# Performance work log

Hardware: AMD Instinct MI355X
Metric: run time of the kernel (lower is better)

## Reference

```python
import jax, jax.numpy as jnp
import numpy as np
from functools import lru_cache
from jax.scipy.linalg import expm

N_QUBITS = 6
DIM = 2 ** N_QUBITS          # 64
N_PAULI = 4 ** N_QUBITS      # 4096


@lru_cache(maxsize=None)
def _pauli_tensor_np(n_qubits):
    # All n-qubit Pauli strings as dense matrices, ordered base-4
    # (digit 0..3 -> I, X, Y, Z; most-significant digit = first qubit).
    I = np.eye(2, dtype=np.complex64)
    X = np.array([[0, 1], [1, 0]], dtype=np.complex64)
    Y = np.array([[0, -1j], [1j, 0]], dtype=np.complex64)
    Z = np.array([[1, 0], [0, -1]], dtype=np.complex64)
    base = np.stack([I, X, Y, Z])  # [4,2,2]
    T = base
    for _ in range(n_qubits - 1):
        k, d = T.shape[0], T.shape[1]
        T = np.einsum('iab,jcd->ijacbd', T, base).reshape(k * 4, d * 2, d * 2)
    return np.ascontiguousarray(T.astype(np.complex64))  # [4^n, 2^n, 2^n]


def setup_inputs() -> dict:
    key = jax.random.key(0)
    kx, kw, kb = jax.random.split(key, 3)
    x = jax.random.normal(kx, (512, 4000), dtype=jnp.float32)
    weight = jax.random.normal(kw, (4, N_PAULI - 1), dtype=jnp.float32)
    bias = jax.random.normal(kb, (DIM,), dtype=jnp.float32)
    return {"x": x, "weight": weight, "bias": bias}


def reference(x, weight, bias):
    # x: [B, in_dim] float32; weight: [n_reps, 4^n - 1]; bias: [out_dim]
    B, in_dim = x.shape
    n_reps = weight.shape[0]
    out_dim = bias.shape[0]
    P = jnp.asarray(_pauli_tensor_np(N_QUBITS))  # [4096, 64, 64] complex64

    # Pad data coefficients up to the full Pauli basis (identity included).
    xp = jnp.pad(x, ((0, 0), (0, N_PAULI - in_dim))).astype(jnp.complex64)

    # Data-encoding Hamiltonian per sample: H_d[b] = sum_p x[b,p] * P[p]
    Hd = jnp.einsum('bp,pij->bij', xp, P)                       # [B,64,64]
    Ud = jax.vmap(expm)(-1j * Hd)                               # [B,64,64]

    # Trainable Hamiltonians per rep (identity Pauli excluded -> global phase).
    Hp = jnp.einsum('rp,pij->rij', weight.astype(jnp.complex64), P[1:])
    Up = jax.vmap(expm)(-1j * Hp)                               # [R,64,64]

    # Data re-uploading circuit on |0...0>: repeat (U_param @ U_data).
    psi = jnp.zeros((B, DIM), dtype=jnp.complex64).at[:, 0].set(1.0)
    for r in range(n_reps):
        psi = jnp.einsum('bij,bj->bi', Ud, psi)
        psi = jnp.einsum('ij,bj->bi', Up[r], psi)

    # Observables are computational-basis projectors |k><k|, k < out_dim:
    # <psi|O_k|psi> = |psi_k|^2
    probs = (psi[:, :out_dim].real ** 2 + psi[:, :out_dim].imag ** 2)
    return probs.astype(jnp.float32) + bias
```

## Files before the change

### kernel.cpp

```cpp
#include <hip/hip_runtime.h>
#include <math.h>

typedef float2 cplx;
typedef __attribute__((ext_vector_type(8))) short short8v;
typedef __attribute__((ext_vector_type(4))) short short4v;
typedef __attribute__((ext_vector_type(4))) float float4v;

#define TPB 256
#define IN_DIM 4000
#define NREPS 4

#define C3f  0.16666667f
#define C4f  0.041666668f
#define C5f  8.3333333e-3f
#define C6f  1.3888889e-3f
#define C7f  1.9841270e-4f
#define C8f  2.4801587e-5f
#define C9f  2.7557319e-6f
#define C10f 2.7557319e-7f
#define C11f 2.5052108e-8f
#define C12f 2.0876757e-9f
#define C13f 1.6059044e-10f

#define MFMA(A,B,C) __builtin_amdgcn_mfma_f32_16x16x32_bf16((A),(B),(C),0,0,0)


__device__ __forceinline__ int idxSw(int a, int b) {
    return (a << 6) + ((((b >> 3) + a) & 7) << 3) + (b & 7);
}
__device__ __forceinline__ short f2bf(float f) {
    unsigned u = __float_as_uint(f);
    return (short)((u + 0x7FFF + ((u >> 16) & 1)) >> 16);
}
__device__ __forceinline__ float bf2f(short s) {
    return __uint_as_float(((unsigned)(unsigned short)s) << 16);
}

__device__ __forceinline__ void mm_mfma(const short* __restrict__ sh, int li, int q,
                                        int mh, int nh,
                                        float4v* __restrict__ accRR, float4v* __restrict__ accII,
                                        float4v* __restrict__ accRI, float4v* __restrict__ accIR)
{
    #pragma unroll
    for (int ks = 0; ks < 2; ks++) {
        const int ch = ks * 4 + q;
        short8v A[2][4];
        #pragma unroll
        for (int dm = 0; dm < 2; dm++) {
            int r = ((mh * 2 + dm) << 4) + li;
            int off = (r << 6) + (((ch + r) & 7) << 3);
            #pragma unroll
            for (int p = 0; p < 4; p++)
                A[dm][p] = *(const short8v*)(sh + p * 4096 + off);
        }
        #pragma unroll
        for (int dn = 0; dn < 2; dn++) {
            int n = ((nh * 2 + dn) << 4) + li;
            int off = (n << 6) + (((ch + n) & 7) << 3);
            short8v Brh = *(const short8v*)(sh + 16384 + off);
            short8v Brl = *(const short8v*)(sh + 16384 + 4096 + off);
            short8v Bih = *(const short8v*)(sh + 16384 + 8192 + off);
            short8v Bil = *(const short8v*)(sh + 16384 + 12288 + off);
            #pragma unroll
            for (int dm = 0; dm < 2; dm++) {
                int ti = dm * 2 + dn;
                short8v arh = A[dm][0], arl = A[dm][1];
                short8v aih = A[dm][2], ail = A[dm][3];
                accRR[ti] = MFMA(arh, Brh, accRR[ti]);
                accRR[ti] = MFMA(arh, Brl, accRR[ti]);
                accRR[ti] = MFMA(arl, Brh, accRR[ti]);
                accII[ti] = MFMA(aih, Bih, accII[ti]);
                accII[ti] = MFMA(aih, Bil, accII[ti]);
                accII[ti] = MFMA(ail, Bih, accII[ti]);
                accRI[ti] = MFMA(arh, Bih, accRI[ti]);
                accRI[ti] = MFMA(arh, Bil, accRI[ti]);
                accRI[ti] = MFMA(arl, Bih, accRI[ti]);
                accIR[ti] = MFMA(aih, Brh, accIR[ti]);
                accIR[ti] = MFMA(aih, Brl, accIR[ti]);
                accIR[ti] = MFMA(ail, Brh, accIR[ti]);
            }
        }
    }
}

__device__ __forceinline__ void write_row(short* __restrict__ sh, int li, int q,
                                          int mh, int nh,
                                          const float4v* cre, const float4v* cim)
{
    #pragma unroll
    for (int dm = 0; dm < 2; dm++)
    #pragma unroll
    for (int dn = 0; dn < 2; dn++) {
        int ti = dm * 2 + dn;
        int c = ((nh * 2 + dn) << 4) + li;
        #pragma unroll
        for (int reg = 0; reg < 4; reg++) {
            int r = ((mh * 2 + dm) << 4) + q * 4 + reg;
            int off = idxSw(r, c);
            float vr = cre[ti][reg], vi = cim[ti][reg];
            short rh = f2bf(vr); short rl = f2bf(vr - bf2f(rh));
            short ih = f2bf(vi); short il = f2bf(vi - bf2f(ih));
            sh[off] = rh; sh[4096 + off] = rl;
            sh[8192 + off] = ih; sh[12288 + off] = il;
        }
    }
}

__device__ __forceinline__ void write_col(short* __restrict__ sh, int li, int q,
                                          int mh, int nh,
                                          const float4v* cre, const float4v* cim)
{
    #pragma unroll
    for (int dm = 0; dm < 2; dm++)
    #pragma unroll
    for (int dn = 0; dn < 2; dn++) {
        int ti = dm * 2 + dn;
        int c = ((nh * 2 + dn) << 4) + li;
        int k0 = ((mh * 2 + dm) << 4) + q * 4;
        int off = idxSw(c, k0);
        short4v rh, rl, ih, il;
        #pragma unroll
        for (int reg = 0; reg < 4; reg++) {
            float vr = cre[ti][reg], vi = cim[ti][reg];
            short h1 = f2bf(vr); rh[reg] = h1; rl[reg] = f2bf(vr - bf2f(h1));
            short h2 = f2bf(vi); ih[reg] = h2; il[reg] = f2bf(vi - bf2f(h2));
        }
        *(short4v*)(sh + 16384 + off) = rh;
        *(short4v*)(sh + 16384 + 4096 + off) = rl;
        *(short4v*)(sh + 16384 + 8192 + off) = ih;
        *(short4v*)(sh + 16384 + 12288 + off) = il;
    }
}

__device__ __forceinline__ void gather_tile(const short* __restrict__ sh, int li, int q,
                                            int mh, int nh, float4v* bre, float4v* bim)
{
    #pragma unroll
    for (int dm = 0; dm < 2; dm++)
    #pragma unroll
    for (int dn = 0; dn < 2; dn++) {
        int ti = dm * 2 + dn;
        int c = ((nh * 2 + dn) << 4) + li;
        #pragma unroll
        for (int reg = 0; reg < 4; reg++) {
            int r = ((mh * 2 + dm) << 4) + q * 4 + reg;
            int off = idxSw(r, c);
            bre[ti][reg] = bf2f(sh[off]) + bf2f(sh[4096 + off]);
            bim[ti][reg] = bf2f(sh[8192 + off]) + bf2f(sh[12288 + off]);
        }
    }
}

__device__ __forceinline__ void adddiag(float4v* ure, float cI, int li, int q, int mh, int nh)
{
    #pragma unroll
    for (int dm = 0; dm < 2; dm++)
    #pragma unroll
    for (int dn = 0; dn < 2; dn++) {
        if (2 * mh + dm == 2 * nh + dn) {
            #pragma unroll
            for (int e = 0; e < 4; e++)
                if (li == q * 4 + e) ure[dm * 2 + dn][e] += cI;
        }
    }
}

__device__ __forceinline__ void pauli_masks(int p, int& xm, int& zm) {
    xm = 0; zm = 0;
    #pragma unroll
    for (int k = 0; k < 6; k++) {
        int lo = (p >> (2 * k)) & 1;
        int hi = (p >> (2 * k + 1)) & 1;
        zm |= hi << k;
        xm |= (hi ^ lo) << k;
    }
}
__device__ __forceinline__ cplx pauli_phase(float v, int xm, int zm) {
    int ny = __popc(xm & zm) & 3;
    if (ny == 0) return make_float2(v, 0.f);
    if (ny == 1) return make_float2(0.f, -v);
    if (ny == 2) return make_float2(-v, 0.f);
    return make_float2(0.f, v);
}

__global__ __launch_bounds__(TPB) void expm_mfma_kernel(const float* __restrict__ x,
                                                        const float* __restrict__ w,
                                                        cplx* __restrict__ ws, int B)
{
    __shared__ float4 LDSf4[4160];
    char* LDS = (char*)LDSf4;
    cplx* W = (cplx*)LDS;
    short* sh = (short*)LDS;
    float* red = (float*)(LDS + 65536);
    int t = threadIdx.x, blk = blockIdx.x;

    float sumsq = 0.f;
    {
        const bool isW = (blk >= B);
        const float* src = isW ? (w + (size_t)(blk - B) * 4095)
                               : (x + (size_t)blk * IN_DIM);
        #pragma unroll
        for (int n = 0; n < 16; n++) {
            int p = t + TPB * n;
            float v = isW ? ((p == 0) ? 0.f : src[p - 1])
                          : ((p < IN_DIM) ? src[p] : 0.f);
            sumsq += v * v;
            int xm, zm; pauli_masks(p, xm, zm);
            W[(xm << 6) + zm] = pauli_phase(v, xm, zm);
        }
    }
    __syncthreads();

    red[t] = sumsq; __syncthreads();
    for (int off = 128; off >= 1; off >>= 1) { if (t < off) red[t] += red[t + off]; __syncthreads(); }
    float fro = sqrtf(64.f * red[0]);
    __syncthreads();
    int s1 = 0; { float nn = fro; while (nn > 8.f && s1 < 24) { nn *= 0.5f; s1++; } }
    float sc1 = exp2f((float)(-s1));

    for (int st = 0; st < 6; st++) {
        int len = 1 << st;
        #pragma unroll
        for (int n = 0; n < 8; n++) {
            int qq = t + TPB * n;
            int m = qq >> 5, bf = qq & 31;
            int lo = bf & (len - 1), hi = bf >> st;
            int z0 = (hi << (st + 1)) | lo, z1 = z0 | len;
            cplx a = W[(m << 6) + z0], b = W[(m << 6) + z1];
            W[(m << 6) + z0] = make_float2(a.x + b.x, a.y + b.y);
            W[(m << 6) + z1] = make_float2(a.x - b.x, a.y - b.y);
        }
        __syncthreads();
    }

    cplx hv[16];
    #pragma unroll
    for (int n = 0; n < 16; n++) hv[n] = W[t + TPB * n];
    __syncthreads();
    #pragma unroll
    for (int n = 0; n < 16; n++) {
        int idx = t + TPB * n;
        int m = idx >> 6, i = idx & 63;
        float vr = hv[n].y * sc1, vi = -hv[n].x * sc1;
        int r = i, c = i ^ m;
        short rh = f2bf(vr), rl = f2bf(vr - bf2f(rh));
        short ih = f2bf(vi), il = f2bf(vi - bf2f(ih));
        int offY = idxSw(r, c);
        int offX = idxSw(c, r);
        sh[offY] = rh; sh[4096 + offY] = rl; sh[8192 + offY] = ih; sh[12288 + offY] = il;
        sh[16384 + offX] = rh; sh[16384 + 4096 + offX] = rl;
        sh[16384 + 8192 + offX] = ih; sh[16384 + 12288 + offX] = il;
    }
    __syncthreads();

    const int lane = t & 63, wv = t >> 6, li = lane & 15, q = lane >> 4;
    const int mh = wv & 1, nh = wv >> 1;
    const float4v z4 = {0.f, 0.f, 0.f, 0.f};
    float4v accRR[4], accII[4], accRI[4], accIR[4];
    float4v ure[4], uim[4];

    #define ZERO_ACC  _Pragma("unroll") for (int i2 = 0; i2 < 4; i2++) { accRR[i2]=z4; accII[i2]=z4; accRI[i2]=z4; accIR[i2]=z4; }

    ZERO_ACC
    mm_mfma(sh, li, q, mh, nh, accRR, accII, accRI, accIR);
    float ss = 0.f;
    #pragma unroll
    for (int ti = 0; ti < 4; ti++) {
        ure[ti] = accRR[ti] - accII[ti];
        uim[ti] = accRI[ti] + accIR[ti];
        #pragma unroll
        for (int e = 0; e < 4; e++) ss += ure[ti][e]*ure[ti][e] + uim[ti][e]*uim[ti][e];
    }
    __syncthreads();

    red[t] = ss; __syncthreads();
    for (int off = 128; off >= 1; off >>= 1) { if (t < off) red[t] += red[t + off]; __syncthreads(); }
    float bound = sqrtf(sqrtf(red[0]));
    int ds = 0; { float nn = bound; while (nn > 2.f && ds < 12) { nn *= 0.5f; ds++; } }
    const int s = s1 + ds;
    float dsc = exp2f((float)(-ds)), dsc2 = dsc * dsc;

    float4v bre[4] = {z4, z4, z4, z4}, bim[4] = {z4, z4, z4, z4};
    gather_tile(sh, li, q, mh, nh, bre, bim);

    #pragma unroll
    for (int ti = 0; ti < 4; ti++) { ure[ti] *= dsc2; uim[ti] *= dsc2; }
    write_col(sh, li, q, mh, nh, ure, uim);
    __syncthreads();

    {
        float ca = C13f * dsc;
        #pragma unroll
        for (int ti = 0; ti < 4; ti++) { ure[ti] = ca * bre[ti]; uim[ti] = ca * bim[ti]; }
        adddiag(ure, C12f, li, q, mh, nh);
        write_row(sh, li, q, mh, nh, ure, uim);
    }
    __syncthreads();

    const float cIc[6] = { 1.0f, 0.5f, C4f, C6f, C8f, C10f };
    const float cAc[6] = { 1.0f, C3f,  C5f, C7f, C9f, C11f };
    #pragma unroll
    for (int j = 5; j >= 0; j--) {
        ZERO_ACC
        mm_mfma(sh, li, q, mh, nh, accRR, accII, accRI, accIR);
        __syncthreads();
        float ca = cAc[j] * dsc, cI = cIc[j];
        #pragma unroll
        for (int ti = 0; ti < 4; ti++) {
            ure[ti] = accRR[ti] - accII[ti] + ca * bre[ti];
            uim[ti] = accRI[ti] + accIR[ti] + ca * bim[ti];
        }
        adddiag(ure, cI, li, q, mh, nh);
        write_row(sh, li, q, mh, nh, ure, uim);
        if (j == 0) write_col(sh, li, q, mh, nh, ure, uim);
        __syncthreads();
    }

    for (int sq = 0; sq < s; sq++) {
        ZERO_ACC
        mm_mfma(sh, li, q, mh, nh, accRR, accII, accRI, accIR);
        __syncthreads();
        #pragma unroll
        for (int ti = 0; ti < 4; ti++) {
            ure[ti] = accRR[ti] - accII[ti];
            uim[ti] = accRI[ti] + accIR[ti];
        }
        if (sq < s - 1) {
            write_row(sh, li, q, mh, nh, ure, uim);
            write_col(sh, li, q, mh, nh, ure, uim);
            __syncthreads();
        }
    }
    #undef ZERO_ACC

    cplx* dst = ws + ((size_t)blk << 12);
    #pragma unroll
    for (int dm = 0; dm < 2; dm++)
    #pragma unroll
    for (int dn = 0; dn < 2; dn++) {
        int ti = dm * 2 + dn;
        int c = ((nh * 2 + dn) << 4) + li;
        int cs = c ^ (((c >> 4) & 1) << 1);
        #pragma unroll
        for (int reg = 0; reg < 4; reg++) {
            int r = ((mh * 2 + dm) << 4) + q * 4 + reg;
            dst[(r << 6) + cs] = make_float2(ure[ti][reg], uim[ti][reg]);
        }
    }
}

__device__ __forceinline__ cplx matvec_row(const cplx* __restrict__ M,
                                           const cplx* __restrict__ pin, int i)
{
    float ax = 0.f, ay = 0.f;
    const float4* Mr = (const float4*)(M + (i << 6));
    #pragma unroll
    for (int mm = 0; mm < 16; mm++) {
        int ch = (mm + (i & 15)) & 15;
        int b = (ch >> 2) & 1;
        float4 m01 = Mr[(ch << 1) + b];
        float4 m23 = Mr[(ch << 1) + 1 - b];
        const cplx* p = pin + (ch << 2);
        cplx p0 = p[0], p1 = p[1], p2 = p[2], p3 = p[3];
        ax = fmaf(m01.x, p0.x, fmaf(-m01.y, p0.y, ax));
        ay = fmaf(m01.x, p0.y, fmaf( m01.y, p0.x, ay));
        ax = fmaf(m01.z, p1.x, fmaf(-m01.w, p1.y, ax));
        ay = fmaf(m01.z, p1.y, fmaf( m01.w, p1.x, ay));
        ax = fmaf(m23.x, p2.x, fmaf(-m23.y, p2.y, ax));
        ay = fmaf(m23.x, p2.y, fmaf( m23.y, p2.x, ay));
        ax = fmaf(m23.z, p3.x, fmaf(-m23.w, p3.y, ax));
        ay = fmaf(m23.z, p3.y, fmaf( m23.w, p3.x, ay));
    }
    return make_float2(ax, ay);
}

__global__ __launch_bounds__(TPB) void matvec_kernel(const cplx* __restrict__ ws,
                                                     const float* __restrict__ bias,
                                                     float* __restrict__ out, int B)
{
    __shared__ float4 Xs4[2048];
    __shared__ float4 Ys4[2048];
    __shared__ cplx psiA[64], psiB[64];
    cplx* X = (cplx*)Xs4;
    cplx* Y = (cplx*)Ys4;
    int t = threadIdx.x, b = blockIdx.x;
    {
        const float4* src = (const float4*)(ws + ((size_t)b << 12));
        float4* dst = (float4*)X;
        #pragma unroll
        for (int n = 0; n < 8; n++) dst[n * TPB + t] = src[n * TPB + t];
    }
    if (t < 64) psiA[t] = make_float2(t == 0 ? 1.f : 0.f, 0.f);
    __syncthreads();
    for (int r = 0; r < NREPS; r++) {
        const float4* src = (const float4*)(ws + ((size_t)(B + r) << 12));
        float4* dstY = (float4*)Y;
        #pragma unroll
        for (int n = 0; n < 8; n++) dstY[n * TPB + t] = src[n * TPB + t];
        __syncthreads();
        if (t < 64) psiB[t] = matvec_row(X, psiA, t);
        __syncthreads();
        if (t < 64) psiA[t] = matvec_row(Y, psiB, t);
        __syncthreads();
    }
    if (t < 64) {
        cplx pv = psiA[t];
        out[(b << 6) + t] = fmaf(pv.x, pv.x, fmaf(pv.y, pv.y, bias[t]));
    }
}

extern "C" void kernel_launch(void* const* d_in, const int* in_sizes, int n_in,
                              void* d_out, int out_size, void* d_ws, size_t ws_size,
                              hipStream_t stream)
{
    const float* x    = (const float*)d_in[0];
    const float* w    = (const float*)d_in[1];
    const float* bias = (const float*)d_in[2];
    float* out = (float*)d_out;
    cplx* ws   = (cplx*)d_ws;

    int B = in_sizes[0] / IN_DIM;

    hipLaunchKernelGGL(expm_mfma_kernel, dim3(B + NREPS), dim3(TPB), 0, stream, x, w, ws, B);
    hipLaunchKernelGGL(matvec_kernel,    dim3(B),         dim3(TPB), 0, stream, ws, bias, out, B);
}
```

Before: 166.1 us.

## Halve MFMA accumulators, shuffle-based transforms, higher-order Taylor, split matvec

Complex matmul now uses two accumulators instead of four by negating the bf16 operands through sign-bit flips, so real and imaginary parts come straight out of the MFMA chains. The Walsh-Hadamard transform and the block reductions move from LDS with many barriers to wave shuffles. The Taylor series is extended to degree 15 with a looser scaling threshold so fewer squarings are needed, at the cost of one more Horner step. LDS is split into separate A and B buffers, and the matvec kernel spreads each row over four waves with a partial-sum reduction instead of using only 64 threads.

```diff
diff --git a/kernel.cpp b/kernel.cpp
--- a/kernel.cpp
+++ b/kernel.cpp
@@ -10,6 +10,9 @@
 #define IN_DIM 4000
 #define NREPS 4
 
+#define C0f  1.0f
+#define C1f  1.0f
+#define C2f  0.5f
 #define C3f  0.16666667f
 #define C4f  0.041666668f
 #define C5f  8.3333333e-3f
@@ -21,6 +24,8 @@
 #define C11f 2.5052108e-8f
 #define C12f 2.0876757e-9f
 #define C13f 1.6059044e-10f
+#define C14f 1.1470746e-11f
+#define C15f 7.6471637e-13f
 
 #define MFMA(A,B,C) __builtin_amdgcn_mfma_f32_16x16x32_bf16((A),(B),(C),0,0,0)
 
@@ -35,55 +40,65 @@
 __device__ __forceinline__ float bf2f(short s) {
     return __uint_as_float(((unsigned)(unsigned short)s) << 16);
 }
-
-__device__ __forceinline__ void mm_mfma(const short* __restrict__ sh, int li, int q,
-                                        int mh, int nh,
-                                        float4v* __restrict__ accRR, float4v* __restrict__ accII,
-                                        float4v* __restrict__ accRI, float4v* __restrict__ accIR)
+__device__ __forceinline__ short8v neg8(short8v a) {
+    int4 u; __builtin_memcpy(&u, &a, 16);
+    u.x ^= 0x80008000; u.y ^= 0x80008000; u.z ^= 0x80008000; u.w ^= 0x80008000;
+    short8v r; __builtin_memcpy(&r, &u, 16); return r;
+}
+
+template<int MODE>
+__device__ __forceinline__ void mm_mfma(const short* __restrict__ As,
+                                        const short* __restrict__ Bs,
+                                        int li, int q, int mh, int nh,
+                                        float4v* __restrict__ accR,
+                                        float4v* __restrict__ accI)
 {
     #pragma unroll
     for (int ks = 0; ks < 2; ks++) {
         const int ch = ks * 4 + q;
-        short8v A[2][4];
+        short8v arh[2], arl[2], aih[2], ail[2], nih[2], nil_[2];
         #pragma unroll
         for (int dm = 0; dm < 2; dm++) {
             int r = ((mh * 2 + dm) << 4) + li;
             int off = (r << 6) + (((ch + r) & 7) << 3);
-            #pragma unroll
-            for (int p = 0; p < 4; p++)
-                A[dm][p] = *(const short8v*)(sh + p * 4096 + off);
+            arh[dm] = *(const short8v*)(As + off);
+            arl[dm] = *(const short8v*)(As + 4096 + off);
+            aih[dm] = *(const short8v*)(As + 8192 + off);
+            ail[dm] = *(const short8v*)(As + 12288 + off);
+            nih[dm] = neg8(aih[dm]);
+            nil_[dm] = neg8(ail[dm]);
         }
         #pragma unroll
         for (int dn = 0; dn < 2; dn++) {
             int n = ((nh * 2 + dn) << 4) + li;
             int off = (n << 6) + (((ch + n) & 7) << 3);
-            short8v Brh = *(const short8v*)(sh + 16384 + off);
-            short8v Brl = *(const short8v*)(sh + 16384 + 4096 + off);
-            short8v Bih = *(const short8v*)(sh + 16384 + 8192 + off);
-            short8v Bil = *(const short8v*)(sh + 16384 + 12288 + off);
+            short8v brh = *(const short8v*)(Bs + off);
+            short8v brl = *(const short8v*)(Bs + 4096 + off);
+            short8v bih = *(const short8v*)(Bs + 8192 + off);
+            short8v bil = *(const short8v*)(Bs + 12288 + off);
+            if (MODE == 1) { brh = neg8(brh); brl = neg8(brl); }
+            if (MODE == 2) { bih = neg8(bih); bil = neg8(bil); }
             #pragma unroll
             for (int dm = 0; dm < 2; dm++) {
                 int ti = dm * 2 + dn;
-                short8v arh = A[dm][0], arl = A[dm][1];
-                short8v aih = A[dm][2], ail = A[dm][3];
-                accRR[ti] = MFMA(arh, Brh, accRR[ti]);
-                accRR[ti] = MFMA(arh, Brl, accRR[ti]);
-                accRR[ti] = MFMA(arl, Brh, accRR[ti]);
-                accII[ti] = MFMA(aih, Bih, accII[ti]);
-                accII[ti] = MFMA(aih, Bil, accII[ti]);
-                accII[ti] = MFMA(ail, Bih, accII[ti]);
-                accRI[ti] = MFMA(arh, Bih, accRI[ti]);
-                accRI[ti] = MFMA(arh, Bil, accRI[ti]);
-                accRI[ti] = MFMA(arl, Bih, accRI[ti]);
-                accIR[ti] = MFMA(aih, Brh, accIR[ti]);
-                accIR[ti] = MFMA(aih, Brl, accIR[ti]);
-                accIR[ti] = MFMA(ail, Brh, accIR[ti]);
+                accR[ti] = MFMA(arh[dm], brh, accR[ti]);
+                accR[ti] = MFMA(arh[dm], brl, accR[ti]);
+                accR[ti] = MFMA(arl[dm], brh, accR[ti]);
+                accR[ti] = MFMA(nih[dm], bih, accR[ti]);
+                accR[ti] = MFMA(nih[dm], bil, accR[ti]);
+                accR[ti] = MFMA(nil_[dm], bih, accR[ti]);
+                accI[ti] = MFMA(arh[dm], bih, accI[ti]);
+                accI[ti] = MFMA(arh[dm], bil, accI[ti]);
+                accI[ti] = MFMA(arl[dm], bih, accI[ti]);
+                accI[ti] = MFMA(aih[dm], brh, accI[ti]);
+                accI[ti] = MFMA(aih[dm], brl, accI[ti]);
+                accI[ti] = MFMA(ail[dm], brh, accI[ti]);
             }
         }
     }
 }
 
-__device__ __forceinline__ void write_row(short* __restrict__ sh, int li, int q,
+__device__ __forceinline__ void write_row(short* __restrict__ S, int li, int q,
                                           int mh, int nh,
                                           const float4v* cre, const float4v* cim)
 {
@@ -98,17 +113,16 @@
             int r = ((mh * 2 + dm) << 4) + q * 4 + reg;
             int off = idxSw(r, c);
             float vr = cre[ti][reg], vi = cim[ti][reg];
-            short rh = f2bf(vr); short rl = f2bf(vr - bf2f(rh));
-            short ih = f2bf(vi); short il = f2bf(vi - bf2f(ih));
-            sh[off] = rh; sh[4096 + off] = rl;
-            sh[8192 + off] = ih; sh[12288 + off] = il;
-        }
-    }
-}
-
-__device__ __forceinline__ void write_col(short* __restrict__ sh, int li, int q,
-                                          int mh, int nh,
-                                          const float4v* cre, const float4v* cim)
+            short rh = f2bf(vr), rl = f2bf(vr - bf2f(rh));
+            short ih = f2bf(vi), il = f2bf(vi - bf2f(ih));
+            S[off] = rh; S[4096 + off] = rl; S[8192 + off] = ih; S[12288 + off] = il;
+        }
+    }
+}
+
+__device__ __forceinline__ void write_rowT(short* __restrict__ S, int li, int q,
+                                           int mh, int nh,
+                                           const float4v* cre, const float4v* cim)
 {
     #pragma unroll
     for (int dm = 0; dm < 2; dm++)
@@ -125,14 +139,14 @@
             short h1 = f2bf(vr); rh[reg] = h1; rl[reg] = f2bf(vr - bf2f(h1));
             short h2 = f2bf(vi); ih[reg] = h2; il[reg] = f2bf(vi - bf2f(h2));
         }
-        *(short4v*)(sh + 16384 + off) = rh;
-        *(short4v*)(sh + 16384 + 4096 + off) = rl;
-        *(short4v*)(sh + 16384 + 8192 + off) = ih;
-        *(short4v*)(sh + 16384 + 12288 + off) = il;
-    }
-}
-
-__device__ __forceinline__ void gather_tile(const short* __restrict__ sh, int li, int q,
+        *(short4v*)(S + off) = rh;
+        *(short4v*)(S + 4096 + off) = rl;
+        *(short4v*)(S + 8192 + off) = ih;
+        *(short4v*)(S + 12288 + off) = il;
+    }
+}
+
+__device__ __forceinline__ void gather_tile(const short* __restrict__ S, int li, int q,
                                             int mh, int nh, float4v* bre, float4v* bim)
 {
     #pragma unroll
@@ -145,8 +159,8 @@
         for (int reg = 0; reg < 4; reg++) {
             int r = ((mh * 2 + dm) << 4) + q * 4 + reg;
             int off = idxSw(r, c);
-            bre[ti][reg] = bf2f(sh[off]) + bf2f(sh[4096 + off]);
-            bim[ti][reg] = bf2f(sh[8192 + off]) + bf2f(sh[12288 + off]);
+            bre[ti][reg] = bf2f(S[off]) + bf2f(S[4096 + off]);
+            bim[ti][reg] = bf2f(S[8192 + off]) + bf2f(S[12288 + off]);
         }
     }
 }
@@ -187,12 +201,14 @@
                                                         const float* __restrict__ w,
                                                         cplx* __restrict__ ws, int B)
 {
-    __shared__ float4 LDSf4[4160];
+    __shared__ float4 LDSf4[4098];
     char* LDS = (char*)LDSf4;
-    cplx* W = (cplx*)LDS;
-    short* sh = (short*)LDS;
+    short* S0 = (short*)LDS;
+    short* S1 = S0 + 16384;
+    cplx* W = (cplx*)(LDS + 32768);
     float* red = (float*)(LDS + 65536);
-    int t = threadIdx.x, blk = blockIdx.x;
+    const int t = threadIdx.x, blk = blockIdx.x;
+    const int lane = t & 63, wv = t >> 6;
 
     float sumsq = 0.f;
     {
@@ -208,126 +224,113 @@
             int xm, zm; pauli_masks(p, xm, zm);
             W[(xm << 6) + zm] = pauli_phase(v, xm, zm);
         }
-    }
-    __syncthreads();
-
-    red[t] = sumsq; __syncthreads();
-    for (int off = 128; off >= 1; off >>= 1) { if (t < off) red[t] += red[t + off]; __syncthreads(); }
-    float fro = sqrtf(64.f * red[0]);
-    __syncthreads();
+        #pragma unroll
+        for (int d = 32; d >= 1; d >>= 1) sumsq += __shfl_xor(sumsq, d, 64);
+        if (lane == 0) red[wv] = sumsq;
+    }
+    __syncthreads();
+
+    float fro = sqrtf(64.f * (red[0] + red[1] + red[2] + red[3]));
     int s1 = 0; { float nn = fro; while (nn > 8.f && s1 < 24) { nn *= 0.5f; s1++; } }
     float sc1 = exp2f((float)(-s1));
 
-    for (int st = 0; st < 6; st++) {
-        int len = 1 << st;
-        #pragma unroll
-        for (int n = 0; n < 8; n++) {
-            int qq = t + TPB * n;
-            int m = qq >> 5, bf = qq & 31;
-            int lo = bf & (len - 1), hi = bf >> st;
-            int z0 = (hi << (st + 1)) | lo, z1 = z0 | len;
-            cplx a = W[(m << 6) + z0], b = W[(m << 6) + z1];
-            W[(m << 6) + z0] = make_float2(a.x + b.x, a.y + b.y);
-            W[(m << 6) + z1] = make_float2(a.x - b.x, a.y - b.y);
-        }
-        __syncthreads();
-    }
-
     cplx hv[16];
     #pragma unroll
-    for (int n = 0; n < 16; n++) hv[n] = W[t + TPB * n];
-    __syncthreads();
-    #pragma unroll
-    for (int n = 0; n < 16; n++) {
-        int idx = t + TPB * n;
-        int m = idx >> 6, i = idx & 63;
-        float vr = hv[n].y * sc1, vi = -hv[n].x * sc1;
-        int r = i, c = i ^ m;
+    for (int rr = 0; rr < 16; rr++) hv[rr] = W[(((wv << 4) + rr) << 6) + lane];
+    #pragma unroll
+    for (int d = 1; d < 64; d <<= 1) {
+        float sg = (lane & d) ? -1.f : 1.f;
+        #pragma unroll
+        for (int rr = 0; rr < 16; rr++) {
+            float px = __shfl_xor(hv[rr].x, d, 64);
+            float py = __shfl_xor(hv[rr].y, d, 64);
+            hv[rr].x = fmaf(sg, hv[rr].x, px);
+            hv[rr].y = fmaf(sg, hv[rr].y, py);
+        }
+    }
+    __syncthreads();
+
+    #pragma unroll
+    for (int rr = 0; rr < 16; rr++) {
+        int m = (wv << 4) + rr;
+        int c = lane ^ m;
+        float vr = hv[rr].y * sc1, vi = -hv[rr].x * sc1;
         short rh = f2bf(vr), rl = f2bf(vr - bf2f(rh));
         short ih = f2bf(vi), il = f2bf(vi - bf2f(ih));
-        int offY = idxSw(r, c);
-        int offX = idxSw(c, r);
-        sh[offY] = rh; sh[4096 + offY] = rl; sh[8192 + offY] = ih; sh[12288 + offY] = il;
-        sh[16384 + offX] = rh; sh[16384 + 4096 + offX] = rl;
-        sh[16384 + 8192 + offX] = ih; sh[16384 + 12288 + offX] = il;
-    }
-    __syncthreads();
-
-    const int lane = t & 63, wv = t >> 6, li = lane & 15, q = lane >> 4;
+        int off = idxSw(lane, c);
+        S0[off] = rh; S0[4096 + off] = rl; S0[8192 + off] = ih; S0[12288 + off] = il;
+    }
+    __syncthreads();
+
+    const int li = lane & 15, q = lane >> 4;
     const int mh = wv & 1, nh = wv >> 1;
     const float4v z4 = {0.f, 0.f, 0.f, 0.f};
-    float4v accRR[4], accII[4], accRI[4], accIR[4];
-    float4v ure[4], uim[4];
-
-    #define ZERO_ACC  _Pragma("unroll") for (int i2 = 0; i2 < 4; i2++) { accRR[i2]=z4; accII[i2]=z4; accRI[i2]=z4; accIR[i2]=z4; }
+    float4v accR[4], accI[4];
+    #define ZERO_ACC _Pragma("unroll") for (int i2 = 0; i2 < 4; i2++) { accR[i2]=z4; accI[i2]=z4; }
 
     ZERO_ACC
-    mm_mfma(sh, li, q, mh, nh, accRR, accII, accRI, accIR);
+    mm_mfma<1>(S0, S0, li, q, mh, nh, accR, accI);
     float ss = 0.f;
     #pragma unroll
-    for (int ti = 0; ti < 4; ti++) {
-        ure[ti] = accRR[ti] - accII[ti];
-        uim[ti] = accRI[ti] + accIR[ti];
-        #pragma unroll
-        for (int e = 0; e < 4; e++) ss += ure[ti][e]*ure[ti][e] + uim[ti][e]*uim[ti][e];
-    }
-    __syncthreads();
-
-    red[t] = ss; __syncthreads();
-    for (int off = 128; off >= 1; off >>= 1) { if (t < off) red[t] += red[t + off]; __syncthreads(); }
-    float bound = sqrtf(sqrtf(red[0]));
-    int ds = 0; { float nn = bound; while (nn > 2.f && ds < 12) { nn *= 0.5f; ds++; } }
+    for (int ti = 0; ti < 4; ti++)
+        #pragma unroll
+        for (int e = 0; e < 4; e++)
+            ss += accR[ti][e]*accR[ti][e] + accI[ti][e]*accI[ti][e];
+    #pragma unroll
+    for (int d = 32; d >= 1; d >>= 1) ss += __shfl_xor(ss, d, 64);
+    if (lane == 0) red[4 + wv] = ss;
+    __syncthreads();
+
+    float bound = sqrtf(sqrtf(red[4] + red[5] + red[6] + red[7]));
+    int ds = 0; { float nn = bound; while (nn > 3.4f && ds < 12) { nn *= 0.5f; ds++; } }
     const int s = s1 + ds;
     float dsc = exp2f((float)(-ds)), dsc2 = dsc * dsc;
 
-    float4v bre[4] = {z4, z4, z4, z4}, bim[4] = {z4, z4, z4, z4};
-    gather_tile(sh, li, q, mh, nh, bre, bim);
-
-    #pragma unroll
-    for (int ti = 0; ti < 4; ti++) { ure[ti] *= dsc2; uim[ti] *= dsc2; }
-    write_col(sh, li, q, mh, nh, ure, uim);
-    __syncthreads();
-
+    float4v bre[4], bim[4];
+    gather_tile(S0, li, q, mh, nh, bre, bim);
+    __syncthreads();
+
+    float4v ure[4], uim[4];
+    #pragma unroll
+    for (int ti = 0; ti < 4; ti++) { ure[ti] = accR[ti] * dsc2; uim[ti] = accI[ti] * dsc2; }
+    write_row(S1, li, q, mh, nh, ure, uim);
     {
-        float ca = C13f * dsc;
+        float ca = C15f * dsc;
         #pragma unroll
         for (int ti = 0; ti < 4; ti++) { ure[ti] = ca * bre[ti]; uim[ti] = ca * bim[ti]; }
-        adddiag(ure, C12f, li, q, mh, nh);
-        write_row(sh, li, q, mh, nh, ure, uim);
-    }
-    __syncthreads();
-
-    const float cIc[6] = { 1.0f, 0.5f, C4f, C6f, C8f, C10f };
-    const float cAc[6] = { 1.0f, C3f,  C5f, C7f, C9f, C11f };
-    #pragma unroll
-    for (int j = 5; j >= 0; j--) {
+        adddiag(ure, C14f, li, q, mh, nh);
+        write_row(S0, li, q, mh, nh, ure, uim);
+    }
+    __syncthreads();
+
+    const float cIc[7] = { C0f, C2f, C4f, C6f, C8f, C10f, C12f };
+    const float cAc[7] = { C1f, C3f, C5f, C7f, C9f, C11f, C13f };
+    for (int j = 6; j >= 0; j--) {
         ZERO_ACC
-        mm_mfma(sh, li, q, mh, nh, accRR, accII, accRI, accIR);
+        mm_mfma<2>(S0, S1, li, q, mh, nh, accR, accI);
         __syncthreads();
         float ca = cAc[j] * dsc, cI = cIc[j];
         #pragma unroll
         for (int ti = 0; ti < 4; ti++) {
-            ure[ti] = accRR[ti] - accII[ti] + ca * bre[ti];
-            uim[ti] = accRI[ti] + accIR[ti] + ca * bim[ti];
+            ure[ti] = accR[ti] + ca * bre[ti];
+            uim[ti] = accI[ti] + ca * bim[ti];
         }
         adddiag(ure, cI, li, q, mh, nh);
-        write_row(sh, li, q, mh, nh, ure, uim);
-        if (j == 0) write_col(sh, li, q, mh, nh, ure, uim);
-        __syncthreads();
-    }
-
+        write_row(S0, li, q, mh, nh, ure, uim);
+        __syncthreads();
+    }
+
+    write_rowT(S1, li, q, mh, nh, ure, uim);
+    __syncthreads();
     for (int sq = 0; sq < s; sq++) {
         ZERO_ACC
-        mm_mfma(sh, li, q, mh, nh, accRR, accII, accRI, accIR);
-        __syncthreads();
-        #pragma unroll
-        for (int ti = 0; ti < 4; ti++) {
-            ure[ti] = accRR[ti] - accII[ti];
-            uim[ti] = accRI[ti] + accIR[ti];
-        }
+        mm_mfma<0>(S0, S1, li, q, mh, nh, accR, accI);
+        __syncthreads();
+        #pragma unroll
+        for (int ti = 0; ti < 4; ti++) { ure[ti] = accR[ti]; uim[ti] = accI[ti]; }
         if (sq < s - 1) {
-            write_row(sh, li, q, mh, nh, ure, uim);
-            write_col(sh, li, q, mh, nh, ure, uim);
+            write_row(S0, li, q, mh, nh, ure, uim);
+            write_rowT(S1, li, q, mh, nh, ure, uim);
             __syncthreads();
         }
     }
@@ -349,14 +352,15 @@
     }
 }
 
-__device__ __forceinline__ cplx matvec_row(const cplx* __restrict__ M,
-                                           const cplx* __restrict__ pin, int i)
+__device__ __forceinline__ cplx matvec_partial(const cplx* __restrict__ M,
+                                               const cplx* __restrict__ pin,
+                                               int i, int g)
 {
     float ax = 0.f, ay = 0.f;
     const float4* Mr = (const float4*)(M + (i << 6));
     #pragma unroll
-    for (int mm = 0; mm < 16; mm++) {
-        int ch = (mm + (i & 15)) & 15;
+    for (int c = 0; c < 4; c++) {
+        int ch = ((g << 2) + c + (i & 15)) & 15;
         int b = (ch >> 2) & 1;
         float4 m01 = Mr[(ch << 1) + b];
         float4 m23 = Mr[(ch << 1) + 1 - b];
@@ -381,9 +385,11 @@
     __shared__ float4 Xs4[2048];
     __shared__ float4 Ys4[2048];
     __shared__ cplx psiA[64], psiB[64];
+    __shared__ cplx part[256];
     cplx* X = (cplx*)Xs4;
     cplx* Y = (cplx*)Ys4;
-    int t = threadIdx.x, b = blockIdx.x;
+    const int t = threadIdx.x, b = blockIdx.x;
+    const int i = t & 63, g = t >> 6;
     {
         const float4* src = (const float4*)(ws + ((size_t)b << 12));
         float4* dst = (float4*)X;
@@ -392,15 +398,27 @@
     }
     if (t < 64) psiA[t] = make_float2(t == 0 ? 1.f : 0.f, 0.f);
     __syncthreads();
+
     for (int r = 0; r < NREPS; r++) {
-        const float4* src = (const float4*)(ws + ((size_t)(B + r) << 12));
-        float4* dstY = (float4*)Y;
-        #pragma unroll
-        for (int n = 0; n < 8; n++) dstY[n * TPB + t] = src[n * TPB + t];
-        __syncthreads();
-        if (t < 64) psiB[t] = matvec_row(X, psiA, t);
-        __syncthreads();
-        if (t < 64) psiA[t] = matvec_row(Y, psiB, t);
+        {
+            const float4* src = (const float4*)(ws + ((size_t)(B + r) << 12));
+            float4* dstY = (float4*)Y;
+            #pragma unroll
+            for (int n = 0; n < 8; n++) dstY[n * TPB + t] = src[n * TPB + t];
+        }
+        part[t] = matvec_partial(X, psiA, i, g);
+        __syncthreads();
+        if (t < 64) {
+            cplx a0 = part[t], a1 = part[64 + t], a2 = part[128 + t], a3 = part[192 + t];
+            psiB[t] = make_float2(a0.x + a1.x + a2.x + a3.x, a0.y + a1.y + a2.y + a3.y);
+        }
+        __syncthreads();
+        part[t] = matvec_partial(Y, psiB, i, g);
+        __syncthreads();
+        if (t < 64) {
+            cplx a0 = part[t], a1 = part[64 + t], a2 = part[128 + t], a3 = part[192 + t];
+            psiA[t] = make_float2(a0.x + a1.x + a2.x + a3.x, a0.y + a1.y + a2.y + a3.y);
+        }
         __syncthreads();
     }
     if (t < 64) {
```

Result: faster. 161.1 us (-3.0%).
